# Kernel optimization log

Measured on AMD Instinct MI355X. Metric: run time of the kernel, lower is better.

## Reference

```python
import jax, jax.numpy as jnp
import numpy as np

NEG_INF = -1e30  # stand-in for float('-inf'); avoids inf-inf NaN edge cases, same softmax result


def setup_inputs() -> dict:
    key = jax.random.key(0)
    k1, k2, k3, k4, k5 = jax.random.split(key, 5)
    B, T, C, H = 16, 2048, 200, 64
    x = jax.random.normal(k1, (B, T, C), dtype=jnp.float32)
    # padding mask over key positions, broadcastable to [B, T, T]
    padding_mask = jax.random.randint(k2, (B, 1, T), 0, 2, dtype=jnp.int32)
    # nn.Linear(n_embd, head_size, bias=False) weights, stored as [C, H] so y = x @ W
    Wk = jax.random.normal(k3, (C, H), dtype=jnp.float32) * (C ** -0.5)
    Wq = jax.random.normal(k4, (C, H), dtype=jnp.float32) * (C ** -0.5)
    Wv = jax.random.normal(k5, (C, H), dtype=jnp.float32) * (C ** -0.5)
    return {"x": x, "padding_mask": padding_mask, "Wk": Wk, "Wq": Wq, "Wv": Wv}


def reference(x, padding_mask, Wk, Wq, Wv):
    # x: [B,T,C]; padding_mask: [B,1,T] (0 = padded key position)
    k = x @ Wk  # [B,T,H]
    q = x @ Wq  # [B,T,H]
    v = x @ Wv  # [B,T,H]
    scale = k.shape[-1] ** -0.5
    wei = jnp.einsum("bqh,bkh->bqk", q, k) * scale  # [B,T,T]
    # mask padded key columns before softmax
    wei = jnp.where(padding_mask == 0, NEG_INF, wei)
    wei = jax.nn.softmax(wei, axis=-1)
    # mask padded query rows (transpose of padding mask) to exact zero after softmax
    mask_t = jnp.swapaxes(padding_mask, -2, -1)  # [B,T,1]
    wei = jnp.where(mask_t == 0, 0.0, wei)
    # dropout is identity in eval mode
    out = jnp.einsum("bqk,bkh->bqh", wei, v)  # [B,T,H]
    return out
```

## Files before the change

kernel.cpp:

```cpp
#include <hip/hip_runtime.h>


typedef __attribute__((ext_vector_type(8))) __bf16 bf16x8;
typedef __attribute__((ext_vector_type(4))) __bf16 bf16x4;
typedef __attribute__((ext_vector_type(4))) float f32x4;

#define T_SEQ 2048
#define C_DIM 200
#define H_DIM 64
#define BT_TOT 32768
#define QKV_ELEMS 2097152
#define PPAD 72
#define OPAD 68
#define WTF_FULL 36864
#define WTF_ELEMS 38400
#define LOG2E 1.44269504088896f

__global__ void prep_w(const float* __restrict__ Wk, const float* __restrict__ Wq,
                       const float* __restrict__ Wv, __bf16* __restrict__ WtF) {
    int idx = blockIdx.x * 256 + threadIdx.x;
    if (idx >= WTF_ELEMS) return;
    int w, c, h;
    if (idx < WTF_FULL) {
        int j = idx & 7, lane = (idx >> 3) & 63;
        int chunk = idx >> 9;
        int t = chunk & 3, rest = chunk >> 2;
        w = rest % 3; int ks = rest / 3;
        c = ks * 32 + (lane >> 4) * 8 + j;
        h = t * 16 + (lane & 15);
    } else {
        int i2 = idx - WTF_FULL;
        int j = i2 & 7, l15 = (i2 >> 3) & 15, t = (i2 >> 7) & 3;
        w = i2 >> 9;
        c = 192 + j;
        h = t * 16 + l15;
    }
    const float* W = (w == 0) ? Wq : (w == 1) ? Wk : Wv;
    float val = W[c * H_DIM + h];
    if (w == 0) val *= 0.125f * LOG2E;
    WtF[idx] = (__bf16)val;
}

__global__ __launch_bounds__(256) void qkv_proj(const float* __restrict__ x,
                                                const __bf16* __restrict__ WtF,
                                                __bf16* __restrict__ qb,
                                                __bf16* __restrict__ kb,
                                                __bf16* __restrict__ vT) {
    __shared__ __bf16 Wl[19200];

    const int tid = threadIdx.x;
    const int wave = tid >> 6, lane = tid & 63, l15 = lane & 15, quad = lane >> 4;
    const int rt = blockIdx.x >> 1;
    const int hh = blockIdx.x & 1;
    const int m0b = rt * 64;
    const int row0 = m0b + wave * 16;

    f32x4 acc[3][2] = {};

    #pragma unroll
    for (int i = 0; i < 10; ++i) {
        const int u = i * 256 + tid;
        if (u < 2400) {
            int src;
            if (u < 2304) {
                const int lc = u >> 6, off = u & 63;
                const int ks = lc / 6, r6 = lc % 6;
                const int w = r6 >> 1, tt = r6 & 1;
                src = ((ks * 12 + w * 4 + 2 * hh + tt) << 6) + off;
            } else {
                const int u2 = u - 2304;
                const int w = u2 >> 5, tt = (u2 >> 4) & 1, un = u2 & 15;
                src = (WTF_FULL >> 3) + ((w * 4 + 2 * hh + tt) << 4) + un;
            }
            *(bf16x8*)(Wl + u * 8) = *(const bf16x8*)(WtF + src * 8);
        }
    }
    __syncthreads();

    #pragma unroll
    for (int ks = 0; ks < 7; ++ks) {
        bf16x8 a;
        if (ks < 6 || quad == 0) {
            const float* xr = x + (size_t)(row0 + l15) * C_DIM + ks * 32 + quad * 8;
            const float4 f0 = *(const float4*)xr;
            const float4 f1 = *(const float4*)(xr + 4);
            a[0]=(__bf16)f0.x; a[1]=(__bf16)f0.y; a[2]=(__bf16)f0.z; a[3]=(__bf16)f0.w;
            a[4]=(__bf16)f1.x; a[5]=(__bf16)f1.y; a[6]=(__bf16)f1.z; a[7]=(__bf16)f1.w;
        } else {
            #pragma unroll
            for (int j = 0; j < 8; ++j) a[j] = (__bf16)0.f;
        }
        #pragma unroll
        for (int w = 0; w < 3; ++w)
            #pragma unroll
            for (int tt = 0; tt < 2; ++tt) {
                const int off = (ks < 6) ? (((ks * 6 + w * 2 + tt) << 9) + lane * 8)
                                         : (18432 + ((w * 2 + tt) << 7) + l15 * 8);
                const bf16x8 bf = *(const bf16x8*)(Wl + off);
                acc[w][tt] = __builtin_amdgcn_mfma_f32_16x16x32_bf16(a, bf, acc[w][tt], 0, 0, 0);
            }
    }

    #pragma unroll
    for (int tt = 0; tt < 2; ++tt)
        #pragma unroll
        for (int r = 0; r < 4; ++r) {
            const size_t m = row0 + quad * 4 + r;
            const int h = hh * 32 + tt * 16 + l15;
            qb[m * H_DIM + h] = (__bf16)acc[0][tt][r];
            kb[m * H_DIM + h] = (__bf16)acc[1][tt][r];
        }
    __syncthreads();
    #pragma unroll
    for (int tt = 0; tt < 2; ++tt)
        #pragma unroll
        for (int r = 0; r < 4; ++r)
            Wl[(tt * 16 + l15) * 72 + wave * 16 + quad * 4 + r] = (__bf16)acc[2][tt][r];
    __syncthreads();
    const int bb = m0b >> 11, tloc = m0b & 2047;
    {
        const int seg = tid;
        const int hl = seg >> 3, s8 = seg & 7;
        *(bf16x8*)(vT + ((size_t)bb * H_DIM + hh * 32 + hl) * T_SEQ + tloc + s8 * 8) =
            *(const bf16x8*)(Wl + hl * 72 + s8 * 8);
    }
}

__global__ __launch_bounds__(256, 2) void attn(const __bf16* __restrict__ qb,
                                               const __bf16* __restrict__ kb,
                                               const __bf16* __restrict__ vT,
                                               const int* __restrict__ pm,
                                               float* __restrict__ out) {
    __shared__ __align__(16) char arena[8192 + 36864];
    float* biasS = (float*)arena;

    const int tid = threadIdx.x;
    const int wave = tid >> 6, lane = tid & 63, l15 = lane & 15, quad = lane >> 4;
    const int ks = wave;

    const int flat = blockIdx.y * 32 + blockIdx.x;
    const int xcd = flat & 7, j = flat >> 3;
    const int b = xcd + 8 * (j & 1);
    const int q0 = (j >> 1) * 64;
    const size_t bT = (size_t)b * T_SEQ;

    for (int i = tid; i < 512; i += 256) {
        const int4 p4 = *(const int4*)(pm + bT + i * 4);
        biasS[i * 4 + 0] = p4.x ? 0.f : -1e30f;
        biasS[i * 4 + 1] = p4.y ? 0.f : -1e30f;
        biasS[i * 4 + 2] = p4.z ? 0.f : -1e30f;
        biasS[i * 4 + 3] = p4.w ? 0.f : -1e30f;
    }
    __syncthreads();

    bf16x8 qa[4][2];
    #pragma unroll
    for (int mt = 0; mt < 4; ++mt)
        #pragma unroll
        for (int s = 0; s < 2; ++s)
            qa[mt][s] = *(const bf16x8*)(qb + (bT + q0 + mt * 16 + l15) * H_DIM + s * 32 + quad * 8);

    __bf16* P = (__bf16*)(arena + 8192) + wave * (64 * PPAD);
    const __bf16* kbase = kb + bT * H_DIM;
    const __bf16* vbase = vT + (size_t)b * H_DIM * T_SEQ;

    f32x4 oacc[4][4] = {};
    float lsum[4] = {0.f, 0.f, 0.f, 0.f};

    bf16x8 kf[8];
    #pragma unroll
    for (int n = 0; n < 4; ++n)
        #pragma unroll
        for (int s = 0; s < 2; ++s)
            kf[n * 2 + s] = *(const bf16x8*)(kbase + (ks * 512 + n * 16 + l15) * H_DIM + s * 32 + quad * 8);

    for (int kt = 0; kt < 8; ++kt) {
        const int key0 = ks * 512 + kt * 64;

        bf16x8 vf[8];
        #pragma unroll
        for (int t = 0; t < 4; ++t)
            #pragma unroll
            for (int s = 0; s < 2; ++s)
                vf[t * 2 + s] = *(const bf16x8*)(vbase + (size_t)(t * 16 + l15) * T_SEQ + key0 + s * 32 + quad * 8);

        #pragma unroll
        for (int n = 0; n < 4; ++n) {
            const f32x4 bias = *(const f32x4*)(biasS + key0 + n * 16 + quad * 4);
            f32x4 s_[4];
            #pragma unroll
            for (int mt = 0; mt < 4; ++mt) s_[mt] = bias;
            #pragma unroll
            for (int s = 0; s < 2; ++s)
                #pragma unroll
                for (int mt = 0; mt < 4; ++mt)
                    s_[mt] = __builtin_amdgcn_mfma_f32_16x16x32_bf16(kf[n * 2 + s], qa[mt][s], s_[mt], 0, 0, 0);
            #pragma unroll
            for (int mt = 0; mt < 4; ++mt) {
                bf16x4 p4;
                #pragma unroll
                for (int r = 0; r < 4; ++r) {
                    const float e = exp2f(s_[mt][r]);
                    lsum[mt] += e;
                    p4[r] = (__bf16)e;
                }
                *(bf16x4*)(P + (mt * 16 + l15) * PPAD + n * 16 + quad * 4) = p4;
            }
        }

        const int keyn = ks * 512 + ((kt < 7) ? kt + 1 : 7) * 64;
        #pragma unroll
        for (int n = 0; n < 4; ++n)
            #pragma unroll
            for (int s = 0; s < 2; ++s)
                kf[n * 2 + s] = *(const bf16x8*)(kbase + (keyn + n * 16 + l15) * H_DIM + s * 32 + quad * 8);

        bf16x8 pa[4][2];
        #pragma unroll
        for (int mt = 0; mt < 4; ++mt)
            #pragma unroll
            for (int s = 0; s < 2; ++s)
                pa[mt][s] = *(const bf16x8*)(P + (mt * 16 + l15) * PPAD + s * 32 + quad * 8);

        #pragma unroll
        for (int t = 0; t < 4; ++t)
            #pragma unroll
            for (int s = 0; s < 2; ++s)
                #pragma unroll
                for (int mt = 0; mt < 4; ++mt)
                    oacc[mt][t] = __builtin_amdgcn_mfma_f32_16x16x32_bf16(pa[mt][s], vf[t * 2 + s], oacc[mt][t], 0, 0, 0);
    }

    #pragma unroll
    for (int mt = 0; mt < 4; ++mt) {
        lsum[mt] += __shfl_xor(lsum[mt], 16, 64);
        lsum[mt] += __shfl_xor(lsum[mt], 32, 64);
    }

    float* Ocomb = (float*)(arena + 8192);
    float* Lcomb = Ocomb + 64 * OPAD;

    __syncthreads();
    if (ks == 1) {
        #pragma unroll
        for (int mt = 0; mt < 4; ++mt) {
            #pragma unroll
            for (int t = 0; t < 4; ++t)
                #pragma unroll
                for (int r = 0; r < 4; ++r)
                    Ocomb[(mt * 16 + quad * 4 + r) * OPAD + t * 16 + l15] = oacc[mt][t][r];
            if (quad == 0) Lcomb[mt * 16 + l15] = lsum[mt];
        }
    }
    __syncthreads();
    if (ks == 2) {
        #pragma unroll
        for (int mt = 0; mt < 4; ++mt) {
            #pragma unroll
            for (int t = 0; t < 4; ++t)
                #pragma unroll
                for (int r = 0; r < 4; ++r)
                    Ocomb[(mt * 16 + quad * 4 + r) * OPAD + t * 16 + l15] += oacc[mt][t][r];
            if (quad == 0) Lcomb[mt * 16 + l15] += lsum[mt];
        }
    }
    __syncthreads();
    if (ks == 3) {
        #pragma unroll
        for (int mt = 0; mt < 4; ++mt) {
            #pragma unroll
            for (int t = 0; t < 4; ++t)
                #pragma unroll
                for (int r = 0; r < 4; ++r)
                    Ocomb[(mt * 16 + quad * 4 + r) * OPAD + t * 16 + l15] += oacc[mt][t][r];
            if (quad == 0) Lcomb[mt * 16 + l15] += lsum[mt];
        }
    }
    __syncthreads();
    if (ks == 0) {
        #pragma unroll
        for (int mt = 0; mt < 4; ++mt) {
            lsum[mt] += Lcomb[mt * 16 + l15];
            #pragma unroll
            for (int t = 0; t < 4; ++t)
                #pragma unroll
                for (int r = 0; r < 4; ++r)
                    oacc[mt][t][r] += Ocomb[(mt * 16 + quad * 4 + r) * OPAD + t * 16 + l15];
            #pragma unroll
            for (int r = 0; r < 4; ++r) {
                const int qpos = q0 + mt * 16 + quad * 4 + r;
                const float lv = __shfl(lsum[mt], quad * 4 + r, 64);
                const bool qvalid = biasS[qpos] == 0.f;
                const float inv = (qvalid && lv > 0.f) ? 1.f / lv : 0.f;
                #pragma unroll
                for (int t = 0; t < 4; ++t)
                    out[(bT + qpos) * H_DIM + t * 16 + l15] = oacc[mt][t][r] * inv;
            }
        }
    }
}

extern "C" void kernel_launch(void* const* d_in, const int* in_sizes, int n_in,
                              void* d_out, int out_size, void* d_ws, size_t ws_size,
                              hipStream_t stream) {
    const float* x  = (const float*)d_in[0];
    const int* pm   = (const int*)d_in[1];
    const float* Wk = (const float*)d_in[2];
    const float* Wq = (const float*)d_in[3];
    const float* Wv = (const float*)d_in[4];
    float* out = (float*)d_out;

    __bf16* qb  = (__bf16*)d_ws;
    __bf16* kb  = qb + QKV_ELEMS;
    __bf16* vT  = kb + QKV_ELEMS;
    __bf16* WtF = vT + QKV_ELEMS;

    prep_w<<<dim3((WTF_ELEMS + 255) / 256), dim3(256), 0, stream>>>(Wk, Wq, Wv, WtF);
    qkv_proj<<<dim3(BT_TOT / 64 * 2), dim3(256), 0, stream>>>(x, WtF, qb, kb, vT);
    attn<<<dim3(T_SEQ / 64, 16), dim3(256), 0, stream>>>(qb, kb, vT, pm, out);
}
```

Measured before the change: 127.0 us.

## Read projection weights directly from global memory and prefetch x rows in qkv_proj

The QKV projection kernel no longer stages its 38 KB weight slice into LDS. It reads the pre-swizzled bf16 weights straight from global/L2 and software-prefetches the next x chunk one k-step ahead. Block indices are also remapped so consecutive row tiles spread across the 8 XCDs, and one barrier is dropped. This cuts LDS footprint and the fill-then-sync prologue, which can raise occupancy, at the cost of repeated global/L2 weight loads per wave.

```diff
diff --git a/kernel.cpp b/kernel.cpp
--- a/kernel.cpp
+++ b/kernel.cpp
@@ -46,44 +46,47 @@
                                                 __bf16* __restrict__ qb,
                                                 __bf16* __restrict__ kb,
                                                 __bf16* __restrict__ vT) {
-    __shared__ __bf16 Wl[19200];
+    __shared__ __bf16 Wl[32 * 72];
 
     const int tid = threadIdx.x;
     const int wave = tid >> 6, lane = tid & 63, l15 = lane & 15, quad = lane >> 4;
-    const int rt = blockIdx.x >> 1;
-    const int hh = blockIdx.x & 1;
+    const int flat = blockIdx.x;
+    const int xcd = flat & 7;
+    const int rest = flat >> 3;
+    const int hh = rest & 1;
+    const int rt = (rest >> 1) * 8 + xcd;
     const int m0b = rt * 64;
     const int row0 = m0b + wave * 16;
 
     f32x4 acc[3][2] = {};
 
-    #pragma unroll
-    for (int i = 0; i < 10; ++i) {
-        const int u = i * 256 + tid;
-        if (u < 2400) {
-            int src;
-            if (u < 2304) {
-                const int lc = u >> 6, off = u & 63;
-                const int ks = lc / 6, r6 = lc % 6;
-                const int w = r6 >> 1, tt = r6 & 1;
-                src = ((ks * 12 + w * 4 + 2 * hh + tt) << 6) + off;
-            } else {
-                const int u2 = u - 2304;
-                const int w = u2 >> 5, tt = (u2 >> 4) & 1, un = u2 & 15;
-                src = (WTF_FULL >> 3) + ((w * 4 + 2 * hh + tt) << 4) + un;
+    const float* xrow = x + (size_t)(row0 + l15) * C_DIM;
+
+    float4 f0 = *(const float4*)(xrow + quad * 8);
+    float4 f1 = *(const float4*)(xrow + quad * 8 + 4);
+
+    #pragma unroll 1
+    for (int ks = 0; ks < 6; ++ks) {
+        bf16x8 a;
+        a[0]=(__bf16)f0.x; a[1]=(__bf16)f0.y; a[2]=(__bf16)f0.z; a[3]=(__bf16)f0.w;
+        a[4]=(__bf16)f1.x; a[5]=(__bf16)f1.y; a[6]=(__bf16)f1.z; a[7]=(__bf16)f1.w;
+        if (ks < 5 || quad == 0) {
+            const float* xn = xrow + (ks + 1) * 32 + quad * 8;
+            f0 = *(const float4*)xn;
+            f1 = *(const float4*)(xn + 4);
+        }
+        #pragma unroll
+        for (int w = 0; w < 3; ++w)
+            #pragma unroll
+            for (int tt = 0; tt < 2; ++tt) {
+                const int t4 = w * 4 + 2 * hh + tt;
+                const bf16x8 bf = *(const bf16x8*)(WtF + ((ks * 12 + t4) << 9) + lane * 8);
+                acc[w][tt] = __builtin_amdgcn_mfma_f32_16x16x32_bf16(a, bf, acc[w][tt], 0, 0, 0);
             }
-            *(bf16x8*)(Wl + u * 8) = *(const bf16x8*)(WtF + src * 8);
-        }
-    }
-    __syncthreads();
-
-    #pragma unroll
-    for (int ks = 0; ks < 7; ++ks) {
+    }
+    {
         bf16x8 a;
-        if (ks < 6 || quad == 0) {
-            const float* xr = x + (size_t)(row0 + l15) * C_DIM + ks * 32 + quad * 8;
-            const float4 f0 = *(const float4*)xr;
-            const float4 f1 = *(const float4*)(xr + 4);
+        if (quad == 0) {
             a[0]=(__bf16)f0.x; a[1]=(__bf16)f0.y; a[2]=(__bf16)f0.z; a[3]=(__bf16)f0.w;
             a[4]=(__bf16)f1.x; a[5]=(__bf16)f1.y; a[6]=(__bf16)f1.z; a[7]=(__bf16)f1.w;
         } else {
@@ -94,9 +97,8 @@
         for (int w = 0; w < 3; ++w)
             #pragma unroll
             for (int tt = 0; tt < 2; ++tt) {
-                const int off = (ks < 6) ? (((ks * 6 + w * 2 + tt) << 9) + lane * 8)
-                                         : (18432 + ((w * 2 + tt) << 7) + l15 * 8);
-                const bf16x8 bf = *(const bf16x8*)(Wl + off);
+                const int t4 = w * 4 + 2 * hh + tt;
+                const bf16x8 bf = *(const bf16x8*)(WtF + WTF_FULL + (t4 << 7) + l15 * 8);
                 acc[w][tt] = __builtin_amdgcn_mfma_f32_16x16x32_bf16(a, bf, acc[w][tt], 0, 0, 0);
             }
     }
@@ -110,7 +112,6 @@
             qb[m * H_DIM + h] = (__bf16)acc[0][tt][r];
             kb[m * H_DIM + h] = (__bf16)acc[1][tt][r];
         }
-    __syncthreads();
     #pragma unroll
     for (int tt = 0; tt < 2; ++tt)
         #pragma unroll
```

Result: no change. 126.0 us (-0.8%).
